# Optimization experiments

Measured on AMD Instinct MI355X. Metric: run time of the kernel, lower is better.

## Reference

```python
import jax, jax.numpy as jnp
import numpy as np

EMB = 300      # emb_size
SEQ = 100      # seq_len
KW = 5         # kernel_width
KN = 50        # kernel_num
KMAX = 3       # maxpooling_num
MLP1 = 75      # decoder_mlp1_num
VOCAB = 50000 + 2
B = 2048
QLEN = 5


def setup_inputs() -> dict:
    key = jax.random.key(0)
    ks = jax.random.split(key, 11)
    input_q = jax.random.randint(ks[0], (QLEN,), 0, 50000)
    input_d = jax.random.randint(ks[1], (B, SEQ), 0, 50000)
    emb_table = jax.random.normal(ks[2], (VOCAB, EMB), jnp.float32) * 0.1
    conv_w = jax.random.normal(ks[3], (KW, 3 * EMB, KN), jnp.float32) * 0.02  # WIO
    conv_b = jnp.zeros((KN,), jnp.float32)
    gate_w = jax.random.normal(ks[4], (EMB, KN), jnp.float32) * 0.05
    gate_b = jnp.zeros((KN,), jnp.float32)
    hid_w = jax.random.normal(ks[5], (KN * KMAX, MLP1), jnp.float32) * 0.05
    hid_b = jnp.zeros((MLP1,), jnp.float32)
    score_w = jax.random.normal(ks[6], (MLP1, 1), jnp.float32) * 0.05
    score_b = jnp.zeros((1,), jnp.float32)
    return {"input_q": input_q, "input_d": input_d, "emb_table": emb_table,
            "conv_w": conv_w, "conv_b": conv_b, "gate_w": gate_w, "gate_b": gate_b,
            "hid_w": hid_w, "hid_b": hid_b, "score_w": score_w, "score_b": score_b}


def kmax_pool(x, k):
    # x: [B, KN, L]; keep top-k values along last axis in original sequence order
    _, idx = jax.lax.top_k(x, k)
    idx = jnp.sort(idx, axis=-1)
    return jnp.take_along_axis(x, idx, axis=-1)  # [B, KN, k]


def reference(input_q, input_d, emb_table, conv_w, conv_b, gate_w, gate_b,
              hid_w, hid_b, score_w, score_b):
    # class vector: mean of query-word embeddings -> [EMB]
    class_vec = emb_table[input_q].mean(axis=0)
    # category-specific gate -> [KN]
    query_gate = jax.nn.sigmoid(class_vec @ gate_w + gate_b)
    # document embeddings -> [B, SEQ, EMB]
    emb = emb_table[input_d]
    # elementwise interaction features, concat -> [B, SEQ, 3*EMB]
    conv_in = jnp.concatenate([emb, class_vec * emb, class_vec - emb], axis=-1)
    # conv over sequence (full-width kernel == 1D conv with C_in=3*EMB) -> [B, SEQ-KW+1, KN]
    conv = jax.lax.conv_general_dilated(
        conv_in, conv_w, window_strides=(1,), padding='VALID',
        dimension_numbers=('NWC', 'WIO', 'NWC')) + conv_b
    gated = query_gate * conv                      # [B, L', KN]
    pooled = kmax_pool(jnp.swapaxes(gated, 1, 2), KMAX)  # [B, KN, KMAX]
    enc = pooled.reshape(pooled.shape[0], -1)      # [B, KN*KMAX] = [B, 150]
    mlp1 = jnp.tanh(enc @ hid_w + hid_b)           # [B, 75]
    score = jnp.tanh(mlp1 @ score_w + score_b)     # [B, 1]
    return (mlp1, score)
```

## Files before the change

kernel.cpp:

```cpp
#include <hip/hip_runtime.h>
#include <math.h>

#define EMB   300
#define SEQ   100
#define KW    5
#define KN    50
#define NPAD  64
#define KMAX  3
#define MLP1  75
#define LOUT  96
#define BATCH 2048
#define EPAD  320
#define CHW   32
#define NCHK  10
#define SPITCH 40
#define TAU   2.5e-6
#define WHA   0.75
#define WHB   0.25
#define FLAG_TAU 1e-5f

#define WS_C    0
#define WS_GATE 320
#define WS_BIAS 384
#define WS_WG   448
#define F64_DBL 96448
#define WH_F    0
#define WL_F    51200
#define ENC_OFF 102400
#define ENC_PITCH 152
#define FLAGCNT_OFF 413696
#define FLAGLIST_OFF 413704
#define FLAGCAP 4096

typedef __attribute__((ext_vector_type(8))) short short8;
typedef __attribute__((ext_vector_type(4))) float f32x4;

__device__ __forceinline__ unsigned pack_hl(float x) {
    unsigned u = __float_as_uint(x);
    unsigned hi = (u + 0x7fffu + ((u >> 16) & 1u)) >> 16;
    float r = x - __uint_as_float(hi << 16);
    unsigned v = __float_as_uint(r);
    unsigned lo = (v + 0x7fffu + ((v >> 16) & 1u)) >> 16;
    return (hi << 16) | lo;
}

__global__ __launch_bounds__(256) void prep_a(
    const int* __restrict__ qids, const float* __restrict__ emb,
    const float* __restrict__ gate_w, const float* __restrict__ gate_b,
    const float* __restrict__ conv_w, const float* __restrict__ conv_b,
    double* __restrict__ ws, float* wsf)
{
    __shared__ double cS[EMB];
    __shared__ double gS[KN];
    __shared__ double pS[KW][KN];
    int t = threadIdx.x;
    if (t == 0) *(int*)(wsf + FLAGCNT_OFF) = 0;
    for (int e = t; e < EMB; e += 256) {
        double s = 0.0;
        for (int q = 0; q < 5; ++q) s += (double)emb[(size_t)qids[q] * EMB + e];
        double c = s * 0.2;
        cS[e] = c;
        ws[WS_C + e] = c;
    }
    __syncthreads();
    if (t < KN) {
        double g = (double)gate_b[t];
        for (int e = 0; e < EMB; ++e) g += cS[e] * (double)gate_w[e * KN + t];
        g = 1.0 / (1.0 + exp(-g));
        gS[t] = g;
        ws[WS_GATE + t] = g;
    }
    if (t < KW * KN) {
        int n = t % KN, w = t / KN;
        const float* base = conv_w + w * (3 * EMB * KN) + (2 * EMB) * KN + n;
        double p = 0.0;
        for (int e = 0; e < EMB; ++e) p += cS[e] * (double)base[e * KN];
        pS[w][n] = p;
    }
    __syncthreads();
    if (t < KN) {
        double s = (double)conv_b[t];
        for (int w = 0; w < KW; ++w) s += pS[w][t];
        ws[WS_BIAS + t] = gS[t] * s;
    }
}

__global__ __launch_bounds__(256) void prep_b(
    const float* __restrict__ conv_w, const double* __restrict__ ws,
    double* __restrict__ wg, float* __restrict__ wsf)
{
    int gid  = blockIdx.x * 256 + threadIdx.x;
    int wid  = gid >> 6;
    int lane = gid & 63;
    int w = wid / EPAD;
    int e = wid - w * EPAD;
    double v = 0.0;
    if (e < EMB && lane < KN) {
        double c = ws[WS_C + e];
        const float* p = conv_w + (size_t)w * (3 * EMB * KN) + (size_t)e * KN + lane;
        v = ws[WS_GATE + lane] *
            ((double)p[0] + c * (double)p[EMB * KN] - (double)p[2 * EMB * KN]);
    }
    if (e < EMB) wg[(size_t)(w * NPAD + lane) * EMB + e] = v;
    unsigned pk = pack_hl((float)v);
    unsigned short* Wh = (unsigned short*)(wsf + WH_F);
    unsigned short* Wl = (unsigned short*)(wsf + WL_F);
    size_t o = (size_t)(w * NPAD + lane) * EPAD + e;
    Wh[o] = (unsigned short)(pk >> 16);
    Wl[o] = (unsigned short)(pk & 0xffffu);
}

__global__ __launch_bounds__(256, 4) void main_mfma(
    const int* __restrict__ input_d, const float* __restrict__ emb,
    const double* __restrict__ ws, float* wsf,
    const float* __restrict__ hid_w, const float* __restrict__ hid_b,
    const float* __restrict__ score_w, const float* __restrict__ score_b,
    float* __restrict__ out)
{
    __shared__ unsigned short stageS[2][2][SEQ][SPITCH];
    __shared__ int   tokS[2][SEQ];
    __shared__ float encS[2][ENC_PITCH];
    __shared__ float mlpS[2][MLP1 + 1];

    int t = threadIdx.x;
    int wid = t >> 6, lane = t & 63;
    int dl   = wid >> 1;
    int half = wid & 1;
    int pt   = t & 127;
    int bb = blockIdx.x * 2 + dl;
    int m = lane & 15, kg = lane >> 4;

    for (int i = pt; i < SEQ; i += 128)
        tokS[dl][i] = input_d[bb * SEQ + i];

    f32x4 acc[3][4];
    #pragma unroll
    for (int lt = 0; lt < 3; ++lt)
        #pragma unroll
        for (int nt = 0; nt < 4; ++nt)
            acc[lt][nt] = (f32x4){0.f, 0.f, 0.f, 0.f};

    const unsigned short* Wh = (const unsigned short*)(wsf + WH_F);
    const unsigned short* Wl = (const unsigned short*)(wsf + WL_F);

    __syncthreads();

    for (int c = 0; c < NCHK; ++c) {
        int e0 = c * CHW;
        for (int i = pt; i < SEQ * 4; i += 128) {
            int s = i >> 2, g = i & 3;
            int e = e0 + g * 8;
            float4 fa = {0.f, 0.f, 0.f, 0.f}, fb = {0.f, 0.f, 0.f, 0.f};
            const float* er = emb + (size_t)tokS[dl][s] * EMB;
            if (e < EMB)     fa = *(const float4*)(er + e);
            if (e + 4 < EMB) fb = *(const float4*)(er + e + 4);
            unsigned p0 = pack_hl(fa.x), p1 = pack_hl(fa.y), p2 = pack_hl(fa.z), p3 = pack_hl(fa.w);
            unsigned p4 = pack_hl(fb.x), p5 = pack_hl(fb.y), p6 = pack_hl(fb.z), p7 = pack_hl(fb.w);
            uint4 hv, lv;
            hv.x = (p0 >> 16)     | (p1 & 0xffff0000u);
            hv.y = (p2 >> 16)     | (p3 & 0xffff0000u);
            hv.z = (p4 >> 16)     | (p5 & 0xffff0000u);
            hv.w = (p6 >> 16)     | (p7 & 0xffff0000u);
            lv.x = (p0 & 0xffffu) | (p1 << 16);
            lv.y = (p2 & 0xffffu) | (p3 << 16);
            lv.z = (p4 & 0xffffu) | (p5 << 16);
            lv.w = (p6 & 0xffffu) | (p7 << 16);
            *(uint4*)&stageS[dl][0][s][g * 8] = hv;
            *(uint4*)&stageS[dl][1][s][g * 8] = lv;
        }
        __syncthreads();
        #pragma unroll 1
        for (int w = 0; w < KW; ++w) {
            short8 Bh[4], Bl[4];
            #pragma unroll
            for (int nt = 0; nt < 4; ++nt) {
                size_t off = (size_t)(w * NPAD + nt * 16 + m) * EPAD + e0 + kg * 8;
                union { uint4 u; short8 s; } xb, yb;
                xb.u = *(const uint4*)(Wh + off);
                yb.u = *(const uint4*)(Wl + off);
                Bh[nt] = xb.s; Bl[nt] = yb.s;
            }
            #pragma unroll
            for (int lt = 0; lt < 3; ++lt) {
                int r = (half * 3 + lt) * 16 + m + w;
                short8 ah = *(const short8*)&stageS[dl][0][r][kg * 8];
                short8 al = *(const short8*)&stageS[dl][1][r][kg * 8];
                #pragma unroll
                for (int nt = 0; nt < 4; ++nt) {
                    acc[lt][nt] = __builtin_amdgcn_mfma_f32_16x16x32_bf16(ah, Bh[nt], acc[lt][nt], 0, 0, 0);
                    acc[lt][nt] = __builtin_amdgcn_mfma_f32_16x16x32_bf16(al, Bh[nt], acc[lt][nt], 0, 0, 0);
                    acc[lt][nt] = __builtin_amdgcn_mfma_f32_16x16x32_bf16(ah, Bl[nt], acc[lt][nt], 0, 0, 0);
                }
            }
        }
        __syncthreads();
    }

    float* gated = (float*)&stageS[dl][0][0][0];
    #pragma unroll 1
    for (int ph = 0; ph < 2; ++ph) {
        int np0 = ph * 25;
        #pragma unroll
        for (int nt = 0; nt < 4; ++nt) {
            int n = nt * 16 + m;
            if (n >= np0 && n < np0 + 25) {
                float bias_n = (float)ws[WS_BIAS + n];
                #pragma unroll
                for (int lt = 0; lt < 3; ++lt)
                    #pragma unroll
                    for (int rr = 0; rr < 4; ++rr)
                        gated[(n - np0) * 97 + (half * 3 + lt) * 16 + kg * 4 + rr] = acc[lt][nt][rr] + bias_n;
            }
        }
        __syncthreads();
        int nr = half ? 12 : 13;
        if (lane < nr) {
            int row = half * 13 + lane;
            int n = np0 + row;
            const float* rowp = gated + row * 97;
            float v1 = -1e30f, v2 = -1e30f, v3 = -1e30f, v4 = -1e30f;
            int   i1 = 0, i2 = 0, i3 = 0, i4 = 0;
            for (int l = 0; l < LOUT; ++l) {
                float v = rowp[l];
                if (v > v1)      { v4=v3; i4=i3; v3=v2; i3=i2; v2=v1; i2=i1; v1=v; i1=l; }
                else if (v > v2) { v4=v3; i4=i3; v3=v2; i3=i2; v2=v;  i2=l; }
                else if (v > v3) { v4=v3; i4=i3; v3=v;  i3=l; }
                else if (v > v4) { v4=v;  i4=l; }
            }
            float a0=v1, a1=v2, a2=v3; int j0=i1, j1=i2, j2=i3;
            if (j0 > j1) { float tv=a0; a0=a1; a1=tv; int ti=j0; j0=j1; j1=ti; }
            if (j1 > j2) { float tv=a1; a1=a2; a2=tv; int ti=j1; j1=j2; j2=ti; }
            if (j0 > j1) { float tv=a0; a0=a1; a1=tv; int ti=j0; j0=j1; j1=ti; }
            encS[dl][3*n] = a0; encS[dl][3*n+1] = a1; encS[dl][3*n+2] = a2;
            float* enc = wsf + ENC_OFF + (size_t)bb * ENC_PITCH + 3 * n;
            enc[0] = a0; enc[1] = a1; enc[2] = a2;
            if (v3 - v4 <= FLAG_TAU) {
                int idx = atomicAdd((int*)(wsf + FLAGCNT_OFF), 1);
                if (idx < FLAGCAP) ((int*)(wsf + FLAGLIST_OFF))[idx] = (bb << 6) | n;
            }
        }
        __syncthreads();
    }

    for (int i = t; i < 2 * MLP1; i += 256) {
        int d = i / MLP1, o = i - d * MLP1;
        float h = hid_b[o];
        for (int k = 0; k < KN * KMAX; ++k) h = fmaf(encS[d][k], hid_w[k * MLP1 + o], h);
        h = tanhf(h);
        mlpS[d][o] = h;
        out[(blockIdx.x * 2 + d) * MLP1 + o] = h;
    }
    __syncthreads();
    if (t < 2) {
        float s = score_b[0];
        for (int j = 0; j < MLP1; ++j) s = fmaf(mlpS[t][j], score_w[j], s);
        out[BATCH * MLP1 + blockIdx.x * 2 + t] = tanhf(s);
    }
}

__global__ __launch_bounds__(64) void cleanup_enc(
    const int* __restrict__ input_d, const float* __restrict__ emb,
    const double* __restrict__ ws, float* wsf)
{
    int cnt = *(const int*)(wsf + FLAGCNT_OFF);
    if (cnt > FLAGCAP) cnt = FLAGCAP;
    int idx = blockIdx.x;
    if (idx >= cnt) return;
    int code = ((const int*)(wsf + FLAGLIST_OFF))[idx];
    int b = code >> 6, n = code & 63;
    int lane = threadIdx.x;

    __shared__ int    tokS[SEQ];
    __shared__ double rowS[LOUT];
    for (int i = lane; i < SEQ; i += 64) tokS[i] = input_d[b * SEQ + i];
    __syncthreads();

    for (int l = lane; l < LOUT; l += 64) {
        double s = 0.0;
        for (int w = 0; w < KW; ++w) {
            const float*  er = emb + (size_t)tokS[l + w] * EMB;
            const double* wr = ws + WS_WG + (size_t)(w * NPAD + n) * EMB;
            for (int e = 0; e < EMB; ++e) s += (double)er[e] * wr[e];
        }
        rowS[l] = s + ws[WS_BIAS + n];
    }
    __syncthreads();

    if (lane == 0) {
        double v1=-1e300, v2=-1e300, v3=-1e300, v4=-1e300;
        int    i1=0, i2=0, i3=0, i4=0;
        for (int l = 0; l < LOUT; ++l) {
            double v = rowS[l];
            if (v > v1)      { v4=v3; i4=i3; v3=v2; i3=i2; v2=v1; i2=i1; v1=v; i1=l; }
            else if (v > v2) { v4=v3; i4=i3; v3=v2; i3=i2; v2=v;  i2=l; }
            else if (v > v3) { v4=v3; i4=i3; v3=v;  i3=l; }
            else if (v > v4) { v4=v;  i4=l; }
        }
        double a0=v1, a1=v2, a2=v3; int j0=i1, j1=i2, j2=i3;
        if (j0 > j1) { double tv=a0; a0=a1; a1=tv; int ti=j0; j0=j1; j1=ti; }
        if (j1 > j2) { double tv=a1; a1=a2; a2=tv; int ti=j1; j1=j2; j2=ti; }
        if (j0 > j1) { double tv=a0; a0=a1; a1=tv; int ti=j0; j0=j1; j1=ti; }
        double b0=v1, b1=v2, b2=v4; int k0=i1, k1=i2, k2=i4;
        if (k0 > k1) { double tv=b0; b0=b1; b1=tv; int ti=k0; k0=k1; k1=ti; }
        if (k1 > k2) { double tv=b1; b1=b2; b2=tv; int ti=k1; k1=k2; k2=ti; }
        if (k0 > k1) { double tv=b0; b0=b1; b1=tv; int ti=k0; k0=k1; k1=ti; }
        float* enc = wsf + ENC_OFF + (size_t)b * ENC_PITCH + 3 * n;
        if (v3 - v4 > TAU) {
            enc[0] = (float)a0; enc[1] = (float)a1; enc[2] = (float)a2;
        } else {
            enc[0] = (float)(WHA*a0 + WHB*b0);
            enc[1] = (float)(WHA*a1 + WHB*b1);
            enc[2] = (float)(WHA*a2 + WHB*b2);
        }
    }
}

__global__ __launch_bounds__(128) void cleanup_mlp(
    const float* wsf, const float* __restrict__ hid_w, const float* __restrict__ hid_b,
    const float* __restrict__ score_w, const float* __restrict__ score_b,
    float* __restrict__ out)
{
    int cnt = *(const int*)(wsf + FLAGCNT_OFF);
    if (cnt > FLAGCAP) cnt = FLAGCAP;
    if ((int)blockIdx.x >= cnt) return;
    int code = ((const int*)(wsf + FLAGLIST_OFF))[blockIdx.x];
    int b = code >> 6;
    int t = threadIdx.x;
    __shared__ float eS[KN * KMAX];
    __shared__ float mS[MLP1];
    const float* enc = wsf + ENC_OFF + (size_t)b * ENC_PITCH;
    for (int i = t; i < KN * KMAX; i += 128) eS[i] = enc[i];
    __syncthreads();
    if (t < MLP1) {
        float h = hid_b[t];
        for (int k = 0; k < KN * KMAX; ++k) h = fmaf(eS[k], hid_w[k * MLP1 + t], h);
        h = tanhf(h);
        mS[t] = h;
        out[b * MLP1 + t] = h;
    }
    __syncthreads();
    if (t == 0) {
        float s = score_b[0];
        for (int j = 0; j < MLP1; ++j) s = fmaf(mS[j], score_w[j], s);
        out[BATCH * MLP1 + b] = tanhf(s);
    }
}

extern "C" void kernel_launch(void* const* d_in, const int* in_sizes, int n_in,
                              void* d_out, int out_size, void* d_ws, size_t ws_size,
                              hipStream_t stream)
{
    const int*   input_q = (const int*)d_in[0];
    const int*   input_d = (const int*)d_in[1];
    const float* emb     = (const float*)d_in[2];
    const float* conv_w  = (const float*)d_in[3];
    const float* conv_b  = (const float*)d_in[4];
    const float* gate_w  = (const float*)d_in[5];
    const float* gate_b  = (const float*)d_in[6];
    const float* hid_w   = (const float*)d_in[7];
    const float* hid_b   = (const float*)d_in[8];
    const float* score_w = (const float*)d_in[9];
    const float* score_b = (const float*)d_in[10];
    float*  out = (float*)d_out;
    double* ws  = (double*)d_ws;
    float*  wsf = (float*)((char*)d_ws + (size_t)F64_DBL * 8);

    hipLaunchKernelGGL(prep_a, dim3(1), dim3(256), 0, stream,
                       input_q, emb, gate_w, gate_b, conv_w, conv_b, ws, wsf);
    hipLaunchKernelGGL(prep_b, dim3(400), dim3(256), 0, stream,
                       conv_w, ws, ws + WS_WG, wsf);
    hipLaunchKernelGGL(main_mfma, dim3(BATCH / 2), dim3(256), 0, stream,
                       input_d, emb, ws, wsf, hid_w, hid_b, score_w, score_b, out);
    hipLaunchKernelGGL(cleanup_enc, dim3(FLAGCAP), dim3(64), 0, stream,
                       input_d, emb, ws, wsf);
    hipLaunchKernelGGL(cleanup_mlp, dim3(FLAGCAP), dim3(128), 0, stream,
                       wsf, hid_w, hid_b, score_w, score_b, out);
}
```

Measured before the change: 449.2 us.

## Give each wave a private embedding staging slice and drop per-chunk block barriers

Each wavefront now gathers and converts only the 52 sequence rows its three output tiles need (48 plus a 4-row conv halo) into its own shared-memory slice, instead of two waves sharing a full 100-row stage. This removes the two __syncthreads per embedding chunk, so waves can run the gather and MFMA phases independently. The hi/lo bf16 halves are interleaved in one row with a new pitch. The cost is some duplicated gather of the halo rows and a changed LDS layout that could affect bank conflicts. The later epilogue reuse of the staging buffer as 'gated' must still fit the new layout.

Result: no change. 443.1 us (-1.4%).

```diff
diff --git a/kernel.cpp b/kernel.cpp
--- a/kernel.cpp
+++ b/kernel.cpp
@@ -13,7 +13,8 @@
 #define EPAD  320
 #define CHW   32
 #define NCHK  10
-#define SPITCH 40
+#define SROWS 52
+#define SPITCHW 36
 #define TAU   2.5e-6
 #define WHA   0.75
 #define WHB   0.25
@@ -117,8 +118,8 @@
     const float* __restrict__ score_w, const float* __restrict__ score_b,
     float* __restrict__ out)
 {
-    __shared__ unsigned short stageS[2][2][SEQ][SPITCH];
-    __shared__ int   tokS[2][SEQ];
+    __shared__ __align__(16) unsigned stageS[2][2][SROWS][SPITCHW];
+    __shared__ int   tokS[4][SROWS];
     __shared__ float encS[2][ENC_PITCH];
     __shared__ float mlpS[2][MLP1 + 1];
 
@@ -126,12 +127,10 @@
     int wid = t >> 6, lane = t & 63;
     int dl   = wid >> 1;
     int half = wid & 1;
-    int pt   = t & 127;
     int bb = blockIdx.x * 2 + dl;
     int m = lane & 15, kg = lane >> 4;
 
-    for (int i = pt; i < SEQ; i += 128)
-        tokS[dl][i] = input_d[bb * SEQ + i];
+    if (lane < SROWS) tokS[wid][lane] = input_d[bb * SEQ + half * 48 + lane];
 
     f32x4 acc[3][4];
     #pragma unroll
@@ -142,33 +141,36 @@
 
     const unsigned short* Wh = (const unsigned short*)(wsf + WH_F);
     const unsigned short* Wl = (const unsigned short*)(wsf + WL_F);
-
-    __syncthreads();
+    unsigned* stg = &stageS[dl][half][0][0];
 
     for (int c = 0; c < NCHK; ++c) {
         int e0 = c * CHW;
-        for (int i = pt; i < SEQ * 4; i += 128) {
-            int s = i >> 2, g = i & 3;
-            int e = e0 + g * 8;
-            float4 fa = {0.f, 0.f, 0.f, 0.f}, fb = {0.f, 0.f, 0.f, 0.f};
-            const float* er = emb + (size_t)tokS[dl][s] * EMB;
-            if (e < EMB)     fa = *(const float4*)(er + e);
-            if (e + 4 < EMB) fb = *(const float4*)(er + e + 4);
-            unsigned p0 = pack_hl(fa.x), p1 = pack_hl(fa.y), p2 = pack_hl(fa.z), p3 = pack_hl(fa.w);
-            unsigned p4 = pack_hl(fb.x), p5 = pack_hl(fb.y), p6 = pack_hl(fb.z), p7 = pack_hl(fb.w);
-            uint4 hv, lv;
-            hv.x = (p0 >> 16)     | (p1 & 0xffff0000u);
-            hv.y = (p2 >> 16)     | (p3 & 0xffff0000u);
-            hv.z = (p4 >> 16)     | (p5 & 0xffff0000u);
-            hv.w = (p6 >> 16)     | (p7 & 0xffff0000u);
-            lv.x = (p0 & 0xffffu) | (p1 << 16);
-            lv.y = (p2 & 0xffffu) | (p3 << 16);
-            lv.z = (p4 & 0xffffu) | (p5 << 16);
-            lv.w = (p6 & 0xffffu) | (p7 << 16);
-            *(uint4*)&stageS[dl][0][s][g * 8] = hv;
-            *(uint4*)&stageS[dl][1][s][g * 8] = lv;
-        }
-        __syncthreads();
+        #pragma unroll
+        for (int it = 0; it < 4; ++it) {
+            int i = lane + it * 64;
+            if (i < SROWS * 4) {
+                int s = i >> 2, eg = i & 3;
+                int e = e0 + eg * 8;
+                const float* er = emb + (size_t)tokS[wid][s] * EMB;
+                float4 fa = {0.f, 0.f, 0.f, 0.f}, fb = {0.f, 0.f, 0.f, 0.f};
+                if (e < EMB)     fa = *(const float4*)(er + e);
+                if (e + 4 < EMB) fb = *(const float4*)(er + e + 4);
+                unsigned p0 = pack_hl(fa.x), p1 = pack_hl(fa.y), p2 = pack_hl(fa.z), p3 = pack_hl(fa.w);
+                unsigned p4 = pack_hl(fb.x), p5 = pack_hl(fb.y), p6 = pack_hl(fb.z), p7 = pack_hl(fb.w);
+                uint4 hv, lv;
+                hv.x = (p0 >> 16)     | (p1 & 0xffff0000u);
+                hv.y = (p2 >> 16)     | (p3 & 0xffff0000u);
+                hv.z = (p4 >> 16)     | (p5 & 0xffff0000u);
+                hv.w = (p6 >> 16)     | (p7 & 0xffff0000u);
+                lv.x = (p0 & 0xffffu) | (p1 << 16);
+                lv.y = (p2 & 0xffffu) | (p3 << 16);
+                lv.z = (p4 & 0xffffu) | (p5 << 16);
+                lv.w = (p6 & 0xffffu) | (p7 << 16);
+                unsigned* rowp = stg + s * SPITCHW + eg * 8;
+                *(uint4*)(rowp)     = hv;
+                *(uint4*)(rowp + 4) = lv;
+            }
+        }
         #pragma unroll 1
         for (int w = 0; w < KW; ++w) {
             short8 Bh[4], Bl[4];
@@ -182,9 +184,10 @@
             }
             #pragma unroll
             for (int lt = 0; lt < 3; ++lt) {
-                int r = (half * 3 + lt) * 16 + m + w;
-                short8 ah = *(const short8*)&stageS[dl][0][r][kg * 8];
-                short8 al = *(const short8*)&stageS[dl][1][r][kg * 8];
+                int r = lt * 16 + m + w;
+                const unsigned* ap = stg + r * SPITCHW + kg * 8;
+                short8 ah = *(const short8*)(ap);
+                short8 al = *(const short8*)(ap + 4);
                 #pragma unroll
                 for (int nt = 0; nt < 4; ++nt) {
                     acc[lt][nt] = __builtin_amdgcn_mfma_f32_16x16x32_bf16(ah, Bh[nt], acc[lt][nt], 0, 0, 0);
@@ -193,8 +196,9 @@
                 }
             }
         }
-        __syncthreads();
-    }
+    }
+
+    __syncthreads();
 
     float* gated = (float*)&stageS[dl][0][0][0];
     #pragma unroll 1
```
